# Optimization experiments

Hardware: AMD Instinct MI355X
Metric: run time of the kernel (lower is better)

The kernel has to match this reference:

```python
import jax, jax.numpy as jnp
import numpy as np

V, D, H, L, B, S = 8192, 128, 8, 2, 1, 128
HD = D // H
HID = int(8 * D / 3)
EPS = 1e-6


def setup_inputs() -> dict:
    key = jax.random.key(0)
    ks = jax.random.split(key, 12)
    sc = 0.02
    return {
        "idx": jax.random.randint(ks[0], (B, S), 0, V),
        "w_raw": jax.random.normal(ks[1], (D, V), jnp.float32) * sc,
        "norm1_w": jnp.ones((L, D), jnp.float32),
        "norm2_w": jnp.ones((L, D), jnp.float32),
        "wq": jax.random.normal(ks[2], (L, D, D), jnp.float32) * sc,
        "wk": jax.random.normal(ks[3], (L, D, D), jnp.float32) * sc,
        "wv": jax.random.normal(ks[4], (L, D, D), jnp.float32) * sc,
        "wo": jax.random.normal(ks[5], (L, D, D), jnp.float32) * sc,
        "w1": jax.random.normal(ks[6], (L, D, HID), jnp.float32) * sc,
        "w3": jax.random.normal(ks[7], (L, D, HID), jnp.float32) * sc,
        "w2": jax.random.normal(ks[8], (L, HID, D), jnp.float32) * sc,
        "final_norm_w": jnp.ones((D,), jnp.float32),
    }


def rmsnorm(x, w):
    return x * jax.lax.rsqrt(jnp.mean(x * x, axis=-1, keepdims=True) + EPS) * w


def rope_cos_sin(seqlen, hd):
    inv = 1.0 / (10000.0 ** (jnp.arange(0, hd, 2, dtype=jnp.float32) / hd))
    t = jnp.arange(seqlen, dtype=jnp.float32)
    f = jnp.outer(t, inv)  # (S, hd/2)
    return jnp.cos(f), jnp.sin(f)


def apply_rope(x, cos, sin):
    # x: (B,S,H,HD); interleaved complex pairs as in Llama
    x0, x1 = x[..., 0::2], x[..., 1::2]
    c = cos[None, :, None, :]
    s = sin[None, :, None, :]
    r0 = x0 * c - x1 * s
    r1 = x0 * s + x1 * c
    return jnp.stack([r0, r1], axis=-1).reshape(x.shape)


def forward(idx, w_raw, norm1_w, norm2_w, wq, wk, wv, wo, w1, w2, w3, final_norm_w):
    Wemb = jax.nn.sigmoid(w_raw)                 # (D,V)
    x = Wemb.T[idx]                              # Yoneda one-hot @ W.T == gather -> (B,S,D)
    cos, sin = rope_cos_sin(S, HD)
    causal = jnp.tril(jnp.ones((S, S), bool))[None, None]  # (1,1,S,S)
    scale = 1.0 / jnp.sqrt(jnp.float32(HD))
    for i in range(L):
        # Multi-Universe attention (heads == universes), RoPE, causal SDPA
        h = rmsnorm(x, norm1_w[i])
        q = (h @ wq[i]).reshape(B, S, H, HD)
        k = (h @ wk[i]).reshape(B, S, H, HD)
        v = (h @ wv[i]).reshape(B, S, H, HD)
        q = apply_rope(q, cos, sin)
        k = apply_rope(k, cos, sin)
        scores = jnp.einsum("bihd,bjhd->bhij", q, k) * scale
        scores = jnp.where(causal, scores, jnp.float32(-1e9))
        attn = jax.nn.softmax(scores, axis=-1)
        o = jnp.einsum("bhij,bjhd->bihd", attn, v).reshape(B, S, D) @ wo[i]
        x = x + o
        # SwiGLU FFN
        h2 = rmsnorm(x, norm2_w[i])
        x = x + (jax.nn.silu(h2 @ w1[i]) * (h2 @ w3[i])) @ w2[i]
    x_norm = rmsnorm(x, final_norm_w)
    # Godel-Heyting reachability head
    x_n = x_norm / jnp.linalg.norm(x_norm, axis=-1, keepdims=True)      # (B,S,D)
    v_n = (Wemb / jnp.linalg.norm(Wemb, axis=0, keepdims=True)).T        # (V,D)
    a = x_n[:, :, None, :]                                               # (B,S,1,D)
    b = v_n[None, None, :, :]                                            # (1,1,V,D)
    # strict Godel implication: a => b = 1 if a <= b else b
    imp = jnp.where(a <= b, jnp.float32(1.0), b)                         # (B,S,V,D)
    logits = jnp.clip(imp.mean(axis=-1), 1e-6, 1.0 - 1e-6)               # (B,S,V)
    return logits


def reference(idx, w_raw, norm1_w, norm2_w, wq, wk, wv, wo, w1, w2, w3, final_norm_w):
    return forward(idx, w_raw, norm1_w, norm2_w, wq, wk, wv, wo, w1, w2, w3, final_norm_w)
```

## Files before the change

kernel.cpp:

```cpp
#include <hip/hip_runtime.h>
#include <math.h>

#define V 8192
#define D 128
#define NH 8
#define HD 16
#define SEQ 128
#define HID 341
#define EPS 1e-6f

__device__ __forceinline__ float sigm(float x) { return 1.0f / (1.0f + __expf(-x)); }

__device__ __forceinline__ float block_sum256(float v, float* scratch) {
    #pragma unroll
    for (int m = 32; m > 0; m >>= 1) v += __shfl_xor(v, m);
    if ((threadIdx.x & 63) == 0) scratch[threadIdx.x >> 6] = v;
    __syncthreads();
    float s = (scratch[0] + scratch[1]) + (scratch[2] + scratch[3]);
    __syncthreads();
    return s;
}

__device__ __forceinline__ float block_sum1024(float v, float* scratch) {
    #pragma unroll
    for (int m = 32; m > 0; m >>= 1) v += __shfl_xor(v, m);
    if ((threadIdx.x & 63) == 0) scratch[threadIdx.x >> 6] = v;
    __syncthreads();
    float s = ((scratch[0] + scratch[1]) + (scratch[2] + scratch[3])) +
              ((scratch[4] + scratch[5]) + (scratch[6] + scratch[7])) +
              ((scratch[8] + scratch[9]) + (scratch[10] + scratch[11])) +
              ((scratch[12] + scratch[13]) + (scratch[14] + scratch[15]));
    __syncthreads();
    return s;
}

__global__ __launch_bounds__(256, 1) void k_embed_qkv(
    const int* __restrict__ idx, const float* __restrict__ w_raw,
    const float* __restrict__ wq, const float* __restrict__ wk,
    const float* __restrict__ wv, const float* __restrict__ n1w,
    const float* __restrict__ w1, const float* __restrict__ w3,
    const float* __restrict__ w2, const float* __restrict__ wo,
    float* __restrict__ x, float* __restrict__ q, float* __restrict__ k,
    float* __restrict__ v, float* __restrict__ sink) {
    int t = threadIdx.x;
    if (blockIdx.x >= SEQ) {
        int g = (blockIdx.x - SEQ) * 256 + t;
        float acc = 0.f;
        const float4* p = (const float4*)w_raw;
        for (int i = g; i < 262144; i += 65536) {
            float4 u = p[i];
            acc += u.x + u.y + u.z + u.w;
        }
        p = (const float4*)w1;
        if (g < 21824) { float4 u = p[g]; acc += u.x + u.y + u.z + u.w; }
        p = (const float4*)w3;
        if (g < 21824) { float4 u = p[g]; acc += u.x + u.y + u.z + u.w; }
        p = (const float4*)w2;
        if (g < 21824) { float4 u = p[g]; acc += u.x + u.y + u.z + u.w; }
        p = (const float4*)wq;
        if (g < 8192) { float4 u = p[g]; acc += u.x + u.y + u.z + u.w; }
        p = (const float4*)wk;
        if (g < 8192) { float4 u = p[g]; acc += u.x + u.y + u.z + u.w; }
        p = (const float4*)wv;
        if (g < 8192) { float4 u = p[g]; acc += u.x + u.y + u.z + u.w; }
        p = (const float4*)wo;
        if (g < 8192) { float4 u = p[g]; acc += u.x + u.y + u.z + u.w; }
        if (acc == 1234.5678f) sink[0] = acc;
        return;
    }
    __shared__ float hr[D], qrow[D], krow[D], vpart[2][D], scr[4];
    int s = blockIdx.x;
    int col = t & 127, half = t >> 7, dlo = half * 64;
    float xv = 0.f;
    if (t < 128) xv = sigm(w_raw[t * V + idx[s]]);
    float wpre[128];
    const float* wsel = (t < 128) ? wq : wk;
    #pragma unroll
    for (int d = 0; d < 128; ++d) wpre[d] = wsel[d * D + col];
    float wvpre[64];
    #pragma unroll
    for (int d = 0; d < 64; ++d) wvpre[d] = wv[(dlo + d) * D + col];
    if (t < 128) x[s * D + t] = xv;
    float ss = block_sum256(xv * xv, scr);
    float r = 1.0f / sqrtf(ss * (1.0f / D) + EPS);
    if (t < 128) hr[t] = xv * r * n1w[t];
    __syncthreads();
    float a0 = 0, a1 = 0, a2 = 0, a3 = 0;
    #pragma unroll
    for (int d = 0; d < 128; d += 4) {
        a0 += hr[d] * wpre[d];
        a1 += hr[d + 1] * wpre[d + 1];
        a2 += hr[d + 2] * wpre[d + 2];
        a3 += hr[d + 3] * wpre[d + 3];
    }
    float qk = (a0 + a1) + (a2 + a3);
    float b0 = 0, b1 = 0, b2 = 0, b3 = 0;
    #pragma unroll
    for (int d = 0; d < 64; d += 4) {
        b0 += hr[dlo + d] * wvpre[d];
        b1 += hr[dlo + d + 1] * wvpre[d + 1];
        b2 += hr[dlo + d + 2] * wvpre[d + 2];
        b3 += hr[dlo + d + 3] * wvpre[d + 3];
    }
    vpart[half][col] = (b0 + b1) + (b2 + b3);
    if (t < 128) qrow[col] = qk;
    else krow[col] = qk;
    __syncthreads();
    if (t < 128) {
        v[s * D + t] = vpart[0][t] + vpart[1][t];
        int c = t & (HD - 1);
        int m = c >> 1;
        float fr = (float)s * expf(-(float)m * 1.15129254649702283e+00f);
        float cs = cosf(fr), sn = sinf(fr);
        int base = t & ~1;
        float qe = qrow[base], qod = qrow[base + 1];
        float ke = krow[base], kod = krow[base + 1];
        q[s * D + t] = (c & 1) ? (qe * sn + qod * cs) : (qe * cs - qod * sn);
        k[s * D + t] = (c & 1) ? (ke * sn + kod * cs) : (ke * cs - kod * sn);
    }
}

template <int MODE>
__global__ __launch_bounds__(1024, 4) void k_layer(
    const float* __restrict__ q, const float* __restrict__ kg,
    const float* __restrict__ vg, float* __restrict__ x,
    const float* __restrict__ wo, const float* __restrict__ n2w,
    const float* __restrict__ w1, const float* __restrict__ w3,
    const float* __restrict__ w2, const float* __restrict__ wq,
    const float* __restrict__ wk, const float* __restrict__ wv,
    const float* __restrict__ n1w, float* __restrict__ qo, float* __restrict__ ko,
    float* __restrict__ vo, const float* __restrict__ fw, float* __restrict__ xng) {
    __shared__ float ps[NH][SEQ + 1];
    __shared__ float qs[D], orow[D], h2[D];
    __shared__ float part[8][D];
    __shared__ float afA[HID], afB[HID], af[HID];
    __shared__ float rl[NH];
    __shared__ float scr[16];
    int s = blockIdx.x, t = threadIdx.x;
    int col = t & 127, g8 = t >> 7;
    int jlo = g8 * 16, dlo = g8 * 16;

    float qv = 0.f, xr = 0.f;
    if (t < 128) {
        qv = q[s * D + t];
        xr = x[s * D + t];
        qs[t] = qv;
    }
    __syncthreads();

    {
        const float4* kp = (const float4*)&kg[col * D + g8 * HD];
        float4 k0 = kp[0], k1v = kp[1], k2v = kp[2], k3v = kp[3];
        const float* qh = &qs[g8 * HD];
        float acc = k0.x * qh[0] + k0.y * qh[1] + k0.z * qh[2] + k0.w * qh[3] +
                    k1v.x * qh[4] + k1v.y * qh[5] + k1v.z * qh[6] + k1v.w * qh[7] +
                    k2v.x * qh[8] + k2v.y * qh[9] + k2v.z * qh[10] + k2v.w * qh[11] +
                    k3v.x * qh[12] + k3v.y * qh[13] + k3v.z * qh[14] + k3v.w * qh[15];
        ps[g8][col] = (col <= s) ? acc * 0.25f : 0.f;
    }
    __syncthreads();

    if (t < 512) {
        int h = t >> 6, lane = t & 63;
        float pm = -1e30f;
        for (int j = lane; j <= s; j += 64) pm = fmaxf(pm, ps[h][j]);
        #pragma unroll
        for (int m = 32; m > 0; m >>= 1) pm = fmaxf(pm, __shfl_xor(pm, m));
        float psum = 0.f;
        for (int j = lane; j <= s; j += 64) {
            float e = __expf(ps[h][j] - pm);
            ps[h][j] = e;
            psum += e;
        }
        #pragma unroll
        for (int m = 32; m > 0; m >>= 1) psum += __shfl_xor(psum, m);
        if (lane == 0) rl[h] = 1.0f / psum;
    }
    __syncthreads();

    {
        int h = col >> 4;
        float a0 = 0, a1 = 0, a2 = 0, a3 = 0;
        #pragma unroll
        for (int j = 0; j < 16; j += 4) {
            a0 += ps[h][jlo + j] * vg[(jlo + j) * D + col];
            a1 += ps[h][jlo + j + 1] * vg[(jlo + j + 1) * D + col];
            a2 += ps[h][jlo + j + 2] * vg[(jlo + j + 2) * D + col];
            a3 += ps[h][jlo + j + 3] * vg[(jlo + j + 3) * D + col];
        }
        part[g8][col] = (a0 + a1) + (a2 + a3);
    }
    __syncthreads();
    if (t < 128)
        orow[t] = (((part[0][t] + part[1][t]) + (part[2][t] + part[3][t])) +
                   ((part[4][t] + part[5][t]) + (part[6][t] + part[7][t]))) * rl[t >> 4];
    __syncthreads();

    {
        float a0 = 0, a1 = 0;
        #pragma unroll
        for (int u = 0; u < 16; u += 2) {
            a0 += orow[dlo + u] * wo[(dlo + u) * D + col];
            a1 += orow[dlo + u + 1] * wo[(dlo + u + 1) * D + col];
        }
        part[g8][col] = a0 + a1;
    }
    __syncthreads();
    float xn = 0.f;
    if (t < 128)
        xn = xr + ((part[0][t] + part[1][t]) + (part[2][t] + part[3][t])) +
             ((part[4][t] + part[5][t]) + (part[6][t] + part[7][t]));
    float ss2 = block_sum1024((t < 128) ? xn * xn : 0.f, scr);
    float r2 = 1.0f / sqrtf(ss2 * (1.0f / D) + EPS);
    if (t < 128) h2[t] = xn * r2 * n2w[t];
    __syncthreads();

    if (t < 2 * HID) {
        int mat = t >= HID;
        int c2 = mat ? (t - HID) : t;
        const float* w = mat ? w3 : w1;
        float a0 = 0, a1 = 0, a2 = 0, a3 = 0;
        #pragma unroll 8
        for (int d = 0; d < D; d += 4) {
            a0 += h2[d] * w[d * HID + c2];
            a1 += h2[d + 1] * w[(d + 1) * HID + c2];
            a2 += h2[d + 2] * w[(d + 2) * HID + c2];
            a3 += h2[d + 3] * w[(d + 3) * HID + c2];
        }
        if (mat) afB[c2] = (a0 + a1) + (a2 + a3);
        else afA[c2] = (a0 + a1) + (a2 + a3);
    }
    __syncthreads();
    if (t < HID) {
        float a1v = afA[t];
        af[t] = (a1v / (1.0f + __expf(-a1v))) * afB[t];
    }
    __syncthreads();

    {
        int lo = g8 * 43;
        int hi = (lo + 43 > HID) ? HID : lo + 43;
        float a0 = 0, a1 = 0, a2 = 0, a3 = 0;
        int tt = lo;
        #pragma unroll 8
        for (; tt + 3 < hi; tt += 4) {
            a0 += af[tt] * w2[tt * D + col];
            a1 += af[tt + 1] * w2[(tt + 1) * D + col];
            a2 += af[tt + 2] * w2[(tt + 2) * D + col];
            a3 += af[tt + 3] * w2[(tt + 3) * D + col];
        }
        for (; tt < hi; ++tt) a0 += af[tt] * w2[tt * D + col];
        part[g8][col] = (a0 + a1) + (a2 + a3);
    }
    __syncthreads();
    float x2 = 0.f;
    if (t < 128) {
        x2 = xn + ((part[0][t] + part[1][t]) + (part[2][t] + part[3][t])) +
             ((part[4][t] + part[5][t]) + (part[6][t] + part[7][t]));
        if (MODE == 0) x[s * D + t] = x2;
    }

    float ss = block_sum1024((t < 128) ? x2 * x2 : 0.f, scr);
    float r = 1.0f / sqrtf(ss * (1.0f / D) + EPS);

    if constexpr (MODE == 0) {
        if (t < 128) h2[t] = x2 * r * n1w[t];
        __syncthreads();
        float qk = 0.f;
        if (g8 < 3) {
            const float* wsel = (g8 == 0) ? wq : ((g8 == 1) ? wk : wv);
            float a0 = 0, a1 = 0, a2 = 0, a3 = 0;
            #pragma unroll 8
            for (int d = 0; d < D; d += 4) {
                a0 += h2[d] * wsel[d * D + col];
                a1 += h2[d + 1] * wsel[(d + 1) * D + col];
                a2 += h2[d + 2] * wsel[(d + 2) * D + col];
                a3 += h2[d + 3] * wsel[(d + 3) * D + col];
            }
            qk = (a0 + a1) + (a2 + a3);
        }
        if (g8 == 0) qs[col] = qk;
        else if (g8 == 1) orow[col] = qk;
        else if (g8 == 2) part[0][col] = qk;
        __syncthreads();
        if (t < 128) {
            vo[s * D + t] = part[0][t];
            int c = t & (HD - 1);
            int mm = c >> 1;
            float fr = (float)s * expf(-(float)mm * 1.15129254649702283e+00f);
            float cs = cosf(fr), sn = sinf(fr);
            int base = t & ~1;
            float qe = qs[base], qod = qs[base + 1];
            float ke = orow[base], kod = orow[base + 1];
            qo[s * D + t] = (c & 1) ? (qe * sn + qod * cs) : (qe * cs - qod * sn);
            ko[s * D + t] = (c & 1) ? (ke * sn + kod * cs) : (ke * cs - kod * sn);
        }
    } else {
        float y = (t < 128) ? x2 * r * fw[t] : 0.f;
        float nn = block_sum1024(y * y, scr);
        if (t < 128) xng[t * SEQ + s] = y / sqrtf(nn);
    }
}

__global__ __launch_bounds__(256) void k_logits(const float* __restrict__ xng,
                                                const float* __restrict__ w_raw,
                                                float* __restrict__ out) {
    __shared__ float xs[D * 64];
    __shared__ float vs[D * 32];
    __shared__ float nred[256];
    __shared__ float invn_s[32];
    int t = threadIdx.x;
    int sbase = (blockIdx.x & 1) * 64;
    int vbase = (blockIdx.x >> 1) * 32;
    for (int i = t; i < D * 64; i += 256) {
        int d = i >> 6, s2 = i & 63;
        xs[i] = xng[d * SEQ + sbase + s2];
    }
    for (int i = t; i < D * 32; i += 256) {
        int d = i >> 5, jj = i & 31;
        vs[i] = sigm(w_raw[d * V + vbase + jj]);
    }
    __syncthreads();
    {
        int colc = t & 31, dp = t >> 5;
        float p = 0.f;
        for (int u = 0; u < 16; ++u) {
            float vv = vs[(dp * 16 + u) * 32 + colc];
            p += vv * vv;
        }
        nred[t] = p;
    }
    __syncthreads();
    if (t < 32) {
        float sum = 0.f;
        for (int u = 0; u < 8; ++u) sum += nred[u * 32 + t];
        invn_s[t] = 1.0f / sqrtf(sum);
    }
    __syncthreads();
    for (int i = t; i < D * 32; i += 256) vs[i] *= invn_s[i & 31];
    __syncthreads();
    int vg = t & 15;
    int sg = t >> 4;
    float acc[4][2] = {};
    for (int d = 0; d < D; ++d) {
        float4 xq = *(const float4*)&xs[d * 64 + sg * 4];
        float2 vq = *(const float2*)&vs[d * 32 + vg * 2];
        acc[0][0] += (xq.x <= vq.x) ? 1.0f : vq.x;
        acc[0][1] += (xq.x <= vq.y) ? 1.0f : vq.y;
        acc[1][0] += (xq.y <= vq.x) ? 1.0f : vq.x;
        acc[1][1] += (xq.y <= vq.y) ? 1.0f : vq.y;
        acc[2][0] += (xq.z <= vq.x) ? 1.0f : vq.x;
        acc[2][1] += (xq.z <= vq.y) ? 1.0f : vq.y;
        acc[3][0] += (xq.w <= vq.x) ? 1.0f : vq.x;
        acc[3][1] += (xq.w <= vq.y) ? 1.0f : vq.y;
    }
    const float inv128 = 1.0f / 128.0f;
    #pragma unroll
    for (int si = 0; si < 4; ++si) {
        int s = sbase + sg * 4 + si;
        float2 ov;
        ov.x = fminf(fmaxf(acc[si][0] * inv128, 1e-6f), 1.0f - 1e-6f);
        ov.y = fminf(fmaxf(acc[si][1] * inv128, 1e-6f), 1.0f - 1e-6f);
        *(float2*)&out[s * V + vbase + vg * 2] = ov;
    }
}

extern "C" void kernel_launch(void* const* d_in, const int* in_sizes, int n_in,
                              void* d_out, int out_size, void* d_ws, size_t ws_size,
                              hipStream_t stream) {
    const int* idx = (const int*)d_in[0];
    const float* w_raw = (const float*)d_in[1];
    const float* n1w = (const float*)d_in[2];
    const float* n2w = (const float*)d_in[3];
    const float* wq = (const float*)d_in[4];
    const float* wk = (const float*)d_in[5];
    const float* wv = (const float*)d_in[6];
    const float* wo = (const float*)d_in[7];
    const float* w1 = (const float*)d_in[8];
    const float* w3 = (const float*)d_in[9];
    const float* w2 = (const float*)d_in[10];
    const float* fnw = (const float*)d_in[11];
    float* out = (float*)d_out;
    float* ws = (float*)d_ws;

    float* x    = ws;
    float* q1   = ws + 16384;
    float* k1   = ws + 32768;
    float* v1   = ws + 49152;
    float* q2   = ws + 65536;
    float* k2   = ws + 81920;
    float* v2   = ws + 98304;
    float* xng  = ws + 114688;
    float* sink = ws + 131072;

    k_embed_qkv<<<dim3(SEQ + 256), dim3(256), 0, stream>>>(
        idx, w_raw, wq, wk, wv, n1w, w1, w3, w2, wo, x, q1, k1, v1, sink);
    k_layer<0><<<dim3(SEQ), dim3(1024), 0, stream>>>(
        q1, k1, v1, x, wo, n2w, w1, w3, w2,
        wq + D * D, wk + D * D, wv + D * D, n1w + D, q2, k2, v2,
        (const float*)nullptr, (float*)nullptr);
    k_layer<1><<<dim3(SEQ), dim3(1024), 0, stream>>>(
        q2, k2, v2, x, wo + D * D, n2w + D, w1 + D * HID, w3 + D * HID,
        w2 + HID * D, (const float*)nullptr, (const float*)nullptr,
        (const float*)nullptr, (const float*)nullptr, (float*)nullptr,
        (float*)nullptr, (float*)nullptr, fnw, xng);
    k_logits<<<dim3(512), dim3(256), 0, stream>>>(xng, w_raw, out);
}
```

Baseline: 139.5 us.

## Restructure embed/QKV kernel to 1024-thread blocks with separate Q, K, V thread groups

The embedding and QKV projection kernel now uses 1024-thread blocks. Three 128-thread groups each compute one of Q, K and V over the full 128-wide reduction, reading weights straight from global memory. This replaces the large per-thread register preloads and the split V partial sums. The L2-warming blocks are resized to 128 blocks of 1024 threads and still cover the same weight ranges. The aim is to cut register pressure and simplify the work split, at the cost of leaving five of eight waves idle in the compute blocks and no longer issuing the weight loads before the norm reduction.

```diff
diff --git a/kernel.cpp b/kernel.cpp
--- a/kernel.cpp
+++ b/kernel.cpp
@@ -11,16 +11,6 @@
 
 __device__ __forceinline__ float sigm(float x) { return 1.0f / (1.0f + __expf(-x)); }
 
-__device__ __forceinline__ float block_sum256(float v, float* scratch) {
-    #pragma unroll
-    for (int m = 32; m > 0; m >>= 1) v += __shfl_xor(v, m);
-    if ((threadIdx.x & 63) == 0) scratch[threadIdx.x >> 6] = v;
-    __syncthreads();
-    float s = (scratch[0] + scratch[1]) + (scratch[2] + scratch[3]);
-    __syncthreads();
-    return s;
-}
-
 __device__ __forceinline__ float block_sum1024(float v, float* scratch) {
     #pragma unroll
     for (int m = 32; m > 0; m >>= 1) v += __shfl_xor(v, m);
@@ -34,7 +24,7 @@
     return s;
 }
 
-__global__ __launch_bounds__(256, 1) void k_embed_qkv(
+__global__ __launch_bounds__(1024, 4) void k_embed_qkv(
     const int* __restrict__ idx, const float* __restrict__ w_raw,
     const float* __restrict__ wq, const float* __restrict__ wk,
     const float* __restrict__ wv, const float* __restrict__ n1w,
@@ -44,10 +34,10 @@
     float* __restrict__ v, float* __restrict__ sink) {
     int t = threadIdx.x;
     if (blockIdx.x >= SEQ) {
-        int g = (blockIdx.x - SEQ) * 256 + t;
+        int g = (blockIdx.x - SEQ) * 1024 + t;
         float acc = 0.f;
         const float4* p = (const float4*)w_raw;
-        for (int i = g; i < 262144; i += 65536) {
+        for (int i = g; i < 262144; i += 131072) {
             float4 u = p[i];
             acc += u.x + u.y + u.z + u.w;
         }
@@ -68,46 +58,37 @@
         if (acc == 1234.5678f) sink[0] = acc;
         return;
     }
-    __shared__ float hr[D], qrow[D], krow[D], vpart[2][D], scr[4];
+    __shared__ float hr[D], qrow[D], krow[D], vrow[D], scr[16];
     int s = blockIdx.x;
-    int col = t & 127, half = t >> 7, dlo = half * 64;
+    int col = t & 127, g8 = t >> 7;
     float xv = 0.f;
-    if (t < 128) xv = sigm(w_raw[t * V + idx[s]]);
-    float wpre[128];
-    const float* wsel = (t < 128) ? wq : wk;
-    #pragma unroll
-    for (int d = 0; d < 128; ++d) wpre[d] = wsel[d * D + col];
-    float wvpre[64];
-    #pragma unroll
-    for (int d = 0; d < 64; ++d) wvpre[d] = wv[(dlo + d) * D + col];
-    if (t < 128) x[s * D + t] = xv;
-    float ss = block_sum256(xv * xv, scr);
+    if (t < 128) {
+        xv = sigm(w_raw[t * V + idx[s]]);
+        x[s * D + t] = xv;
+    }
+    float ss = block_sum1024((t < 128) ? xv * xv : 0.f, scr);
     float r = 1.0f / sqrtf(ss * (1.0f / D) + EPS);
     if (t < 128) hr[t] = xv * r * n1w[t];
     __syncthreads();
-    float a0 = 0, a1 = 0, a2 = 0, a3 = 0;
-    #pragma unroll
-    for (int d = 0; d < 128; d += 4) {
-        a0 += hr[d] * wpre[d];
-        a1 += hr[d + 1] * wpre[d + 1];
-        a2 += hr[d + 2] * wpre[d + 2];
-        a3 += hr[d + 3] * wpre[d + 3];
-    }
-    float qk = (a0 + a1) + (a2 + a3);
-    float b0 = 0, b1 = 0, b2 = 0, b3 = 0;
-    #pragma unroll
-    for (int d = 0; d < 64; d += 4) {
-        b0 += hr[dlo + d] * wvpre[d];
-        b1 += hr[dlo + d + 1] * wvpre[d + 1];
-        b2 += hr[dlo + d + 2] * wvpre[d + 2];
-        b3 += hr[dlo + d + 3] * wvpre[d + 3];
-    }
-    vpart[half][col] = (b0 + b1) + (b2 + b3);
-    if (t < 128) qrow[col] = qk;
-    else krow[col] = qk;
+    float qk = 0.f;
+    if (g8 < 3) {
+        const float* wsel = (g8 == 0) ? wq : ((g8 == 1) ? wk : wv);
+        float a0 = 0, a1 = 0, a2 = 0, a3 = 0;
+        #pragma unroll 8
+        for (int d = 0; d < D; d += 4) {
+            a0 += hr[d] * wsel[d * D + col];
+            a1 += hr[d + 1] * wsel[(d + 1) * D + col];
+            a2 += hr[d + 2] * wsel[(d + 2) * D + col];
+            a3 += hr[d + 3] * wsel[(d + 3) * D + col];
+        }
+        qk = (a0 + a1) + (a2 + a3);
+    }
+    if (g8 == 0) qrow[col] = qk;
+    else if (g8 == 1) krow[col] = qk;
+    else if (g8 == 2) vrow[col] = qk;
     __syncthreads();
     if (t < 128) {
-        v[s * D + t] = vpart[0][t] + vpart[1][t];
+        v[s * D + t] = vrow[t];
         int c = t & (HD - 1);
         int m = c >> 1;
         float fr = (float)s * expf(-(float)m * 1.15129254649702283e+00f);
@@ -393,7 +374,7 @@
     float* xng  = ws + 114688;
     float* sink = ws + 131072;
 
-    k_embed_qkv<<<dim3(SEQ + 256), dim3(256), 0, stream>>>(
+    k_embed_qkv<<<dim3(SEQ + 128), dim3(1024), 0, stream>>>(
         idx, w_raw, wq, wk, wv, n1w, w1, w3, w2, wo, x, q1, k1, v1, sink);
     k_layer<0><<<dim3(SEQ), dim3(1024), 0, stream>>>(
         q1, k1, v1, x, wo, n2w, w1, w3, w2,
```

New measurement: 140.2 us (median of 2 runs). No clear change (+0.5%).
